# Kernel tuning notes

Hardware: AMD Instinct MI355X
Metric: run time of the kernel (lower is better)

The kernel has to match this reference:

```python
import jax, jax.numpy as jnp
import numpy as np
import math

B, CIN, COUT, K, R = 8, 128, 128, 7, 2
GC = 16                     # group_channels (init arg `groups`)
G = COUT // GC              # number of dynamic-weight groups = 8
H = W = 32
EPS = 1e-5


def c4_lift(w):
    # w: [o, i, 4] -> dense 1x1 weight [o*4, i*4] via cyclic C4 shifts
    # torch: weight[:, r] = w[..., roll-by-r]  (e.g. r=1 -> [3,0,1,2])
    Wr = jnp.stack([jnp.roll(w, r, axis=-1) for r in range(4)], axis=1)  # [o,4,i,4]
    o, _, i, _ = Wr.shape
    return Wr.reshape(o * 4, i * 4)


def setup_inputs() -> dict:
    key = jax.random.key(0)
    ks = jax.random.split(key, 4)
    sc = 1.0 / math.sqrt(4 * CIN / 2)
    x = jax.random.normal(ks[0], (B, CIN * 4, H, W), dtype=jnp.float32)
    v_w = jax.random.normal(ks[1], (COUT, CIN, 4), dtype=jnp.float32) * sc
    c1_w = jax.random.normal(ks[2], (CIN // R, CIN, 4), dtype=jnp.float32) * sc
    gn_g = jnp.ones((CIN // R * 4,), jnp.float32)
    gn_b = jnp.zeros((CIN // R * 4,), jnp.float32)
    c2_w = jax.random.normal(ks[3], (K * K * G, CIN // R), dtype=jnp.float32) * (1.0 / math.sqrt(CIN // R))
    c2_b = jnp.zeros((K * K * G,), jnp.float32)
    return {"x": x, "v_w": v_w, "c1_w": c1_w, "gn_g": gn_g, "gn_b": gn_b, "c2_w": c2_w, "c2_b": c2_b}


def _forward(x, v_w, c1_w, gn_g, gn_b, c2_w, c2_b):
    b, _, h, w = x.shape
    # conv1: C4-equivariant 1x1
    t = jnp.einsum('oc,bchw->bohw', c4_lift(c1_w), x)        # [b, (CIN//R)*4, h, w]
    # GroupNorm(num_groups=CIN//R) -> normalize each group of 4 channels over (4,h,w)
    tr = t.reshape(b, CIN // R, 4, h, w)
    mu = tr.mean(axis=(2, 3, 4), keepdims=True)
    var = tr.var(axis=(2, 3, 4), keepdims=True)
    t = ((tr - mu) * jax.lax.rsqrt(var + EPS)).reshape(b, CIN // R * 4, h, w)
    t = jax.nn.relu(t * gn_g[None, :, None, None] + gn_b[None, :, None, None])
    # conv2: Conv3d 1x1 over the (c, 4) view
    tv = t.reshape(b, CIN // R, 4, h, w)
    wmap = jnp.einsum('oc,bcrhw->borhw', c2_w, tv) + c2_b[None, :, None, None, None]
    wmap = wmap.reshape(b, G, K, K, 4, h, w)
    # rotate the KxK kernel by r*90deg for C4 element r (r=0 identity)
    wmap = jnp.stack([jnp.rot90(wmap[:, :, :, :, r], k=r, axes=(2, 3)) for r in range(4)], axis=4)
    wmap = wmap.reshape(b, G, K * K, 4, h, w)                 # [b, g, p, r, h, w]
    # v branch (C4 1x1) + unfold (im2col, pad (K-1)//2, stride 1)
    v = jnp.einsum('oc,bchw->bohw', c4_lift(v_w), x)          # [b, COUT*4, h, w]
    p = (K - 1) // 2
    vp = jnp.pad(v, ((0, 0), (0, 0), (p, p), (p, p)))
    patches = jnp.stack([vp[:, :, i:i + h, j:j + w] for i in range(K) for j in range(K)], axis=2)
    patches = patches.reshape(b, G, GC, 4, K * K, h, w)       # [b, g, c, r, p, h, w]
    out = jnp.einsum('bgprhw,bgcrphw->bgcrhw', wmap, patches)
    return out.reshape(b, COUT * 4, h, w)


def reference(x, v_w, c1_w, gn_g, gn_b, c2_w, c2_b):
    return _forward(x, v_w, c1_w, gn_g, gn_b, c2_w, c2_b)
```

## Files before the change

### kernel.cpp

```cpp
#include <hip/hip_runtime.h>

#define BB   8
#define CIN  128
#define COUT 128
#define KS   7
#define HH   32
#define WWID 32
#define HW   1024
#define NG   8
#define GC   16
#define MROWS 768
#define TROWS 256
#define VROWS 512
#define KDIM 512
#define WMAP_O 392
#define WMAP_OP 448
#define C2K  64

#define AS1 __attribute__((address_space(1)))
#define AS3 __attribute__((address_space(3)))

typedef __attribute__((ext_vector_type(8))) short bf16x8;
typedef __attribute__((ext_vector_type(4))) float f32x4;

__device__ __forceinline__ short f2bf(float f) {
    unsigned u = __builtin_bit_cast(unsigned, f);
    u += 0x7fff + ((u >> 16) & 1);
    return (short)(u >> 16);
}
__device__ __forceinline__ float bf2f(unsigned short u) {
    unsigned v = (unsigned)u << 16;
    return __builtin_bit_cast(float, v);
}

__global__ __launch_bounds__(256) void prep_kernel(
    const float* __restrict__ x, const float* __restrict__ v_w,
    const float* __restrict__ c1_w, const float* __restrict__ c2_w,
    const float* __restrict__ c2_b,
    short* __restrict__ XT, short* __restrict__ Wb,
    short* __restrict__ c2wb, float* __restrict__ c2bp,
    float* __restrict__ gnstat)
{
    __shared__ short t[64][66];
    int bx = blockIdx.x, tid = threadIdx.x;
    if (bx < 1024) {
        int b = bx >> 7, c0 = ((bx >> 4) & 7) * 64, n0 = (bx & 15) * 64;
        const float* xb = x + ((size_t)b * KDIM + c0) * HW + n0;
        #pragma unroll
        for (int l = 0; l < 16; ++l) {
            int flat = l * 256 + tid;
            int row = flat >> 6, col = flat & 63;
            t[col][row] = f2bf(xb[(size_t)row * HW + col]);
        }
        __syncthreads();
        short* xt = XT + ((size_t)b * HW + n0) * KDIM + c0;
        #pragma unroll
        for (int l = 0; l < 8; ++l) {
            int u = l * 256 + tid;
            int nrow = u >> 5, cp = (u & 31) * 2;
            short2 v = make_short2(t[nrow][cp], t[nrow][cp + 1]);
            *(short2*)(xt + (size_t)nrow * KDIM + cp) = v;
        }
    } else if (bx < 2560) {
        int idx = (bx - 1024) * 256 + tid;
        int row = idx >> 9, col = idx & 511;
        int i = col >> 2, s = col & 3;
        float val;
        if (row < 256) {
            int o = row >> 2, r = row & 3;
            val = c1_w[(o * CIN + i) * 4 + ((s - r) & 3)];
        } else {
            int ro = row - 256;
            int o = ro >> 2, r = ro & 3;
            val = v_w[(o * CIN + i) * 4 + ((s - r) & 3)];
        }
        Wb[idx] = f2bf(val);
    } else if (bx < 2672) {
        int idx = (bx - 2560) * 256 + tid;
        int o = idx >> 6, k = idx & 63;
        c2wb[idx] = f2bf(o < WMAP_O ? c2_w[o * C2K + k] : 0.f);
        if (idx < WMAP_OP)
            c2bp[idx] = idx < WMAP_O ? c2_b[idx] : 0.f;
    } else {
        *(float4*)(gnstat + tid * 4) = make_float4(0.f, 0.f, 0.f, 0.f);
    }
}

#define GBM 64
#define GBN 128
#define GBK 64
__global__ __launch_bounds__(256) void gemm_mfma_kernel(
    const short* __restrict__ Wb, const short* __restrict__ XT,
    short* __restrict__ tvb, float* __restrict__ gnstat)
{
    __shared__ short As[GBM * GBK];
    __shared__ short Bs[GBN * GBK];
    int b  = blockIdx.z;
    int m0 = blockIdx.y * GBM;
    int n0 = blockIdx.x * GBN;
    int tid = threadIdx.x;
    int lane = tid & 63, wv = tid >> 6;
    int wm = wv & 1, wn = wv >> 1;
    int rl = lane & 15, kg = lane >> 4;
    const short* Ab = Wb + (size_t)m0 * KDIM;
    const short* Bb = XT + ((size_t)b * HW + n0) * KDIM;
    f32x4 acc[2][4] = {};

    for (int k0 = 0; k0 < KDIM; k0 += GBK) {
        #pragma unroll
        for (int l = 0; l < 2; ++l) {
            int c = l * 256 + tid;
            int row = c >> 3, kc = c & 7;
            int kcs = kc ^ (row & 7);
            __builtin_amdgcn_global_load_lds(
                (const AS1 void*)(Ab + (size_t)row * KDIM + k0 + kcs * 8),
                (AS3 void*)(As + (l * 256 + wv * 64) * 8), 16, 0, 0);
        }
        #pragma unroll
        for (int l = 0; l < 4; ++l) {
            int c = l * 256 + tid;
            int row = c >> 3, kc = c & 7;
            int kcs = kc ^ (row & 7);
            __builtin_amdgcn_global_load_lds(
                (const AS1 void*)(Bb + (size_t)row * KDIM + k0 + kcs * 8),
                (AS3 void*)(Bs + (l * 256 + wv * 64) * 8), 16, 0, 0);
        }
        __syncthreads();
        #pragma unroll
        for (int ks = 0; ks < 2; ++ks) {
            bf16x8 af[2], bfr[4];
            #pragma unroll
            for (int mf = 0; mf < 2; ++mf) {
                int row = wm * 32 + mf * 16 + rl;
                af[mf] = *(const bf16x8*)(As + row * GBK + ((ks * 4 + kg) ^ (row & 7)) * 8);
            }
            #pragma unroll
            for (int nf = 0; nf < 4; ++nf) {
                int row = wn * 64 + nf * 16 + rl;
                bfr[nf] = *(const bf16x8*)(Bs + row * GBK + ((ks * 4 + kg) ^ (row & 7)) * 8);
            }
            #pragma unroll
            for (int mf = 0; mf < 2; ++mf)
                #pragma unroll
                for (int nf = 0; nf < 4; ++nf)
                    acc[mf][nf] = __builtin_amdgcn_mfma_f32_16x16x32_bf16(af[mf], bfr[nf], acc[mf][nf], 0, 0, 0);
        }
        __syncthreads();
    }

    short* Cb = tvb + (size_t)b * MROWS * HW;
    #pragma unroll
    for (int mf = 0; mf < 2; ++mf) {
        int rowb = m0 + wm * 32 + mf * 16 + kg * 4;
        #pragma unroll
        for (int nf = 0; nf < 4; ++nf) {
            int col = n0 + wn * 64 + nf * 16 + rl;
            #pragma unroll
            for (int i = 0; i < 4; ++i)
                Cb[(size_t)(rowb + i) * HW + col] = f2bf(acc[mf][nf][i]);
        }
    }

    if (m0 < TROWS) {
        #pragma unroll
        for (int mf = 0; mf < 2; ++mf) {
            float s = 0.f, sq = 0.f;
            #pragma unroll
            for (int nf = 0; nf < 4; ++nf)
                #pragma unroll
                for (int i = 0; i < 4; ++i) {
                    float v = acc[mf][nf][i];
                    s += v; sq += v * v;
                }
            #pragma unroll
            for (int m = 1; m <= 8; m <<= 1) {
                s  += __shfl_xor(s, m);
                sq += __shfl_xor(sq, m);
            }
            if (rl == 0) {
                int grp = (m0 + wm * 32 + mf * 16 + kg * 4) >> 2;
                atomicAdd(&gnstat[(b * 64 + grp) * 2],     s);
                atomicAdd(&gnstat[(b * 64 + grp) * 2 + 1], sq);
            }
        }
    }
}

__global__ __launch_bounds__(256) void tkn2_kernel(
    const short* __restrict__ tvb, const float* __restrict__ gnstat,
    const float* __restrict__ gn_g, const float* __restrict__ gn_b,
    short* __restrict__ tn)
{
    __shared__ short ts[64][72];
    __shared__ float sc[64], sh[64];
    int b4r = blockIdx.x;
    int b = b4r >> 2, r = b4r & 3;
    int hw0 = blockIdx.y * 64;
    int tid = threadIdx.x;
    if (tid < 64) {
        float s   = gnstat[(b * 64 + tid) * 2];
        float sq  = gnstat[(b * 64 + tid) * 2 + 1];
        float mu  = s * (1.f / 4096.f);
        float var = sq * (1.f / 4096.f) - mu * mu;
        float inv = rsqrtf(var + 1e-5f);
        int ch = tid * 4 + r;
        float g = gn_g[ch], bb = gn_b[ch];
        sc[tid] = inv * g;
        sh[tid] = bb - mu * inv * g;
    }
    #pragma unroll
    for (int l = 0; l < 16; ++l) {
        int flat = l * 256 + tid;
        int c = flat >> 6, hw = flat & 63;
        ts[c][hw] = tvb[((size_t)b * MROWS + c * 4 + r) * HW + hw0 + hw];
    }
    __syncthreads();
    #pragma unroll
    for (int l = 0; l < 2; ++l) {
        int u = l * 256 + tid;
        int hw = u >> 3, c0 = (u & 7) * 8;
        bf16x8 v;
        #pragma unroll
        for (int j = 0; j < 8; ++j) {
            float f = bf2f((unsigned short)ts[c0 + j][hw]);
            f = fmaxf(f * sc[c0 + j] + sh[c0 + j], 0.f);
            v[j] = f2bf(f);
        }
        *(bf16x8*)(tn + ((size_t)b4r * HW + hw0 + hw) * C2K + c0) = v;
    }
}

__global__ __launch_bounds__(256) void wmap3_kernel(
    const short* __restrict__ c2wb, const short* __restrict__ tn,
    const float* __restrict__ c2bp, short* __restrict__ wmapB)
{
    __shared__ short smem[64 * 64 + 128 * 64];
    short* As = smem;
    short* Bs = smem + 64 * 64;
    short* Ps = smem;
    int n0  = blockIdx.x * 128;
    int m0  = blockIdx.y * 64;
    int b4r = blockIdx.z;
    int tid = threadIdx.x;
    int lane = tid & 63, wv = tid >> 6;
    int wm = wv & 1, wn = wv >> 1;
    int rl = lane & 15, kg = lane >> 4;
    const short* Bb = tn + ((size_t)b4r * HW + n0) * C2K;

    #pragma unroll
    for (int l = 0; l < 2; ++l) {
        int c = l * 256 + tid;
        int row = c >> 3, kc = c & 7;
        int kcs = kc ^ (row & 7);
        __builtin_amdgcn_global_load_lds(
            (const AS1 void*)(c2wb + (size_t)(m0 + row) * C2K + kcs * 8),
            (AS3 void*)(As + (l * 256 + wv * 64) * 8), 16, 0, 0);
    }
    #pragma unroll
    for (int l = 0; l < 4; ++l) {
        int c = l * 256 + tid;
        int row = c >> 3, kc = c & 7;
        int kcs = kc ^ (row & 7);
        __builtin_amdgcn_global_load_lds(
            (const AS1 void*)(Bb + (size_t)row * C2K + kcs * 8),
            (AS3 void*)(Bs + (l * 256 + wv * 64) * 8), 16, 0, 0);
    }
    __syncthreads();

    f32x4 acc[2][4] = {};
    #pragma unroll
    for (int ks = 0; ks < 2; ++ks) {
        bf16x8 af[2], bfr[4];
        #pragma unroll
        for (int mf = 0; mf < 2; ++mf) {
            int row = wm * 32 + mf * 16 + rl;
            af[mf] = *(const bf16x8*)(As + row * 64 + ((ks * 4 + kg) ^ (row & 7)) * 8);
        }
        #pragma unroll
        for (int nf = 0; nf < 4; ++nf) {
            int row = wn * 64 + nf * 16 + rl;
            bfr[nf] = *(const bf16x8*)(Bs + row * 64 + ((ks * 4 + kg) ^ (row & 7)) * 8);
        }
        #pragma unroll
        for (int mf = 0; mf < 2; ++mf)
            #pragma unroll
            for (int nf = 0; nf < 4; ++nf)
                acc[mf][nf] = __builtin_amdgcn_mfma_f32_16x16x32_bf16(af[mf], bfr[nf], acc[mf][nf], 0, 0, 0);
    }
    __syncthreads();

    #pragma unroll
    for (int mf = 0; mf < 2; ++mf) {
        int rowl = wm * 32 + mf * 16 + kg * 4;
        float bi[4];
        #pragma unroll
        for (int i = 0; i < 4; ++i) bi[i] = c2bp[m0 + rowl + i];
        #pragma unroll
        for (int nf = 0; nf < 4; ++nf) {
            int col = wn * 64 + nf * 16 + rl;
            #pragma unroll
            for (int i = 0; i < 4; ++i)
                Ps[(rowl + i) * 136 + col] = f2bf(acc[mf][nf][i] + bi[i]);
        }
    }
    __syncthreads();

    int row = tid >> 2, segl = tid & 3;
    if (m0 + row < WMAP_O) {
        short* dst = wmapB + (size_t)b4r * WMAP_OP * HW + (size_t)(m0 + row) * HW + n0;
        #pragma unroll
        for (int s2 = 0; s2 < 4; ++s2) {
            int col = segl * 8 + s2 * 32;
            *(bf16x8*)(dst + col) = *(const bf16x8*)(Ps + row * 136 + col);
        }
    }
}

__global__ __launch_bounds__(256, 5) void agg7_kernel(
    const short* __restrict__ tvb, const short* __restrict__ wmapB,
    float* __restrict__ out)
{
    __shared__ float vt[16][10][44];
    int bx = blockIdx.x;
    int b = bx >> 5;
    int g = (bx >> 2) & 7;
    int r = bx & 3;
    int h0  = blockIdx.y * 4;
    int tid = threadIdx.x;
    int w0q = tid & 7, hl = (tid >> 3) & 3, cp = tid >> 5;
    int h = h0 + hl, w0 = w0q * 4;

    int A, Bc, Cc;
    if      (r == 0) { A = 0;  Bc = 7;  Cc = 1;  }
    else if (r == 1) { A = 6;  Bc = -1; Cc = 7;  }
    else if (r == 2) { A = 48; Bc = -7; Cc = -1; }
    else             { A = 42; Bc = 1;  Cc = -7; }

    const short* vpb = tvb + ((size_t)b * MROWS + TROWS) * HW;
    for (int e = tid; e < 480; e += 256) {
        int cc  = e / 30;
        int rem = e - cc * 30;
        int row = rem / 3, q = rem - row * 3;
        int col = (q == 0) ? 0 : (36 + (q - 1) * 4);
        *(float4*)(&vt[cc][row][col]) = make_float4(0.f, 0.f, 0.f, 0.f);
    }
    for (int f = tid; f < 1280; f += 256) {
        int cc  = f / 80;
        int rem = f - cc * 80;
        int row = rem >> 3, q = rem & 7;
        int gh = h0 - 3 + row;
        float4 v4 = make_float4(0.f, 0.f, 0.f, 0.f);
        if (gh >= 0 && gh < HH) {
            int ch = (g * GC + cc) * 4 + r;
            ushort4 u = *(const ushort4*)(vpb + (size_t)ch * HW + gh * WWID + q * 4);
            v4 = make_float4(bf2f(u.x), bf2f(u.y), bf2f(u.z), bf2f(u.w));
        }
        *(float4*)(&vt[cc][row][4 + q * 4]) = v4;
    }
    __syncthreads();

    const short* wmb = wmapB + ((size_t)(b * 4 + r) * WMAP_OP + g * 49) * HW + h * WWID + w0;
    float acc[2][4] = {};
    #pragma unroll
    for (int di = 0; di < 7; ++di) {
        float wrf[7][4];
        #pragma unroll
        for (int dj = 0; dj < 7; ++dj) {
            int porig = A + Bc * di + Cc * dj;
            ushort4 wv = *(const ushort4*)(wmb + (size_t)porig * HW);
            wrf[dj][0] = bf2f(wv.x); wrf[dj][1] = bf2f(wv.y);
            wrf[dj][2] = bf2f(wv.z); wrf[dj][3] = bf2f(wv.w);
        }
        #pragma unroll
        for (int c2 = 0; c2 < 2; ++c2) {
            int hc = cp * 2 + c2;
            const float* rp = &vt[hc][hl + di][w0];
            float4 q0 = *(const float4*)(rp);
            float4 q1 = *(const float4*)(rp + 4);
            float4 q2 = *(const float4*)(rp + 8);
            float win[12] = {q0.x, q0.y, q0.z, q0.w,
                             q1.x, q1.y, q1.z, q1.w,
                             q2.x, q2.y, q2.z, q2.w};
            #pragma unroll
            for (int dj = 0; dj < 7; ++dj)
                #pragma unroll
                for (int px = 0; px < 4; ++px)
                    acc[c2][px] += wrf[dj][px] * win[px + dj + 1];
        }
    }
    #pragma unroll
    for (int c2 = 0; c2 < 2; ++c2) {
        int ch = (g * GC + cp * 2 + c2) * 4 + r;
        float4 o4 = make_float4(acc[c2][0], acc[c2][1], acc[c2][2], acc[c2][3]);
        *(float4*)(out + ((size_t)b * 512 + ch) * HW + h * WWID + w0) = o4;
    }
}

extern "C" void kernel_launch(void* const* d_in, const int* in_sizes, int n_in,
                              void* d_out, int out_size, void* d_ws, size_t ws_size,
                              hipStream_t stream)
{
    const float* x    = (const float*)d_in[0];
    const float* v_w  = (const float*)d_in[1];
    const float* c1_w = (const float*)d_in[2];
    const float* gn_g = (const float*)d_in[3];
    const float* gn_b = (const float*)d_in[4];
    const float* c2_w = (const float*)d_in[5];
    const float* c2_b = (const float*)d_in[6];
    float* out = (float*)d_out;

    char* p = (char*)d_ws;
    short* Wb     = (short*)p;           p += (size_t)MROWS * KDIM * 2;
    short* tvb    = (short*)p;           p += (size_t)BB * MROWS * HW * 2;
    short* wmapB  = (short*)p;           p += (size_t)32 * WMAP_OP * HW * 2;
    short* XT     = (short*)wmapB;
    short* tn     = (short*)p;           p += (size_t)32 * HW * C2K * 2;
    short* c2wb   = (short*)p;           p += (size_t)WMAP_OP * C2K * 2;
    float* c2bp   = (float*)p;           p += (size_t)WMAP_OP * 4;
    float* gnstat = (float*)p;           p += (size_t)512 * 2 * 4;

    prep_kernel     <<<2673, 256, 0, stream>>>(x, v_w, c1_w, c2_w, c2_b, XT, Wb, c2wb, c2bp, gnstat);
    gemm_mfma_kernel<<<dim3(HW / GBN, MROWS / GBM, BB), 256, 0, stream>>>(Wb, XT, tvb, gnstat);
    tkn2_kernel     <<<dim3(32, 16), 256, 0, stream>>>(tvb, gnstat, gn_g, gn_b, tn);
    wmap3_kernel    <<<dim3(HW / 128, WMAP_OP / 64, 32), 256, 0, stream>>>(c2wb, tn, c2bp, wmapB);
    agg7_kernel     <<<dim3(BB * NG * 4, 8), 256, 0, stream>>>(tvb, wmapB, out);
}
```

Measured before the change: 62.68 us.

## Shrink GEMM N tile, stage C via LDS, retile aggregation by channel halves

The GEMM tile shrinks from 128 to 64 columns, which doubles the block count. Its epilogue now stages results through shared memory so each row is written to global memory as coalesced 16-byte vectors instead of scattered 2-byte stores. The aggregation kernel now covers 8 rows by 8 channels per block instead of 4 rows by 16 channels, split over a z dimension. This lowers the halo overhead per row, and each wmap load is reused across fewer channels but over more rows. The cost is an extra LDS round trip and barrier in the GEMM, and more total B-tile traffic from the smaller N tile.

```diff
diff --git a/kernel.cpp b/kernel.cpp
--- a/kernel.cpp
+++ b/kernel.cpp
@@ -87,24 +87,26 @@
 }
 
 #define GBM 64
-#define GBN 128
+#define GBN 64
 #define GBK 64
 __global__ __launch_bounds__(256) void gemm_mfma_kernel(
     const short* __restrict__ Wb, const short* __restrict__ XT,
     short* __restrict__ tvb, float* __restrict__ gnstat)
 {
-    __shared__ short As[GBM * GBK];
-    __shared__ short Bs[GBN * GBK];
+    __shared__ short smem[GBM * GBK + GBN * GBK];
+    short* As = smem;
+    short* Bs = smem + GBM * GBK;
+    short* Ps = smem;
     int b  = blockIdx.z;
     int m0 = blockIdx.y * GBM;
     int n0 = blockIdx.x * GBN;
     int tid = threadIdx.x;
     int lane = tid & 63, wv = tid >> 6;
-    int wm = wv & 1, wn = wv >> 1;
+    int wm = wv & 1, wn = (wv >> 1) & 1;
     int rl = lane & 15, kg = lane >> 4;
     const short* Ab = Wb + (size_t)m0 * KDIM;
     const short* Bb = XT + ((size_t)b * HW + n0) * KDIM;
-    f32x4 acc[2][4] = {};
+    f32x4 acc[2][2] = {};
 
     for (int k0 = 0; k0 < KDIM; k0 += GBK) {
         #pragma unroll
@@ -117,7 +119,7 @@
                 (AS3 void*)(As + (l * 256 + wv * 64) * 8), 16, 0, 0);
         }
         #pragma unroll
-        for (int l = 0; l < 4; ++l) {
+        for (int l = 0; l < 2; ++l) {
             int c = l * 256 + tid;
             int row = c >> 3, kc = c & 7;
             int kcs = kc ^ (row & 7);
@@ -128,37 +130,24 @@
         __syncthreads();
         #pragma unroll
         for (int ks = 0; ks < 2; ++ks) {
-            bf16x8 af[2], bfr[4];
+            bf16x8 af[2], bfr[2];
             #pragma unroll
             for (int mf = 0; mf < 2; ++mf) {
                 int row = wm * 32 + mf * 16 + rl;
                 af[mf] = *(const bf16x8*)(As + row * GBK + ((ks * 4 + kg) ^ (row & 7)) * 8);
             }
             #pragma unroll
-            for (int nf = 0; nf < 4; ++nf) {
-                int row = wn * 64 + nf * 16 + rl;
+            for (int nf = 0; nf < 2; ++nf) {
+                int row = wn * 32 + nf * 16 + rl;
                 bfr[nf] = *(const bf16x8*)(Bs + row * GBK + ((ks * 4 + kg) ^ (row & 7)) * 8);
             }
             #pragma unroll
             for (int mf = 0; mf < 2; ++mf)
                 #pragma unroll
-                for (int nf = 0; nf < 4; ++nf)
+                for (int nf = 0; nf < 2; ++nf)
                     acc[mf][nf] = __builtin_amdgcn_mfma_f32_16x16x32_bf16(af[mf], bfr[nf], acc[mf][nf], 0, 0, 0);
         }
         __syncthreads();
-    }
-
-    short* Cb = tvb + (size_t)b * MROWS * HW;
-    #pragma unroll
-    for (int mf = 0; mf < 2; ++mf) {
-        int rowb = m0 + wm * 32 + mf * 16 + kg * 4;
-        #pragma unroll
-        for (int nf = 0; nf < 4; ++nf) {
-            int col = n0 + wn * 64 + nf * 16 + rl;
-            #pragma unroll
-            for (int i = 0; i < 4; ++i)
-                Cb[(size_t)(rowb + i) * HW + col] = f2bf(acc[mf][nf][i]);
-        }
     }
 
     if (m0 < TROWS) {
@@ -166,7 +155,7 @@
         for (int mf = 0; mf < 2; ++mf) {
             float s = 0.f, sq = 0.f;
             #pragma unroll
-            for (int nf = 0; nf < 4; ++nf)
+            for (int nf = 0; nf < 2; ++nf)
                 #pragma unroll
                 for (int i = 0; i < 4; ++i) {
                     float v = acc[mf][nf][i];
@@ -182,6 +171,29 @@
                 atomicAdd(&gnstat[(b * 64 + grp) * 2],     s);
                 atomicAdd(&gnstat[(b * 64 + grp) * 2 + 1], sq);
             }
+        }
+    }
+
+    #pragma unroll
+    for (int mf = 0; mf < 2; ++mf) {
+        int rowl = wm * 32 + mf * 16 + kg * 4;
+        #pragma unroll
+        for (int nf = 0; nf < 2; ++nf) {
+            int col = wn * 32 + nf * 16 + rl;
+            #pragma unroll
+            for (int i = 0; i < 4; ++i)
+                Ps[(rowl + i) * 68 + col] = f2bf(acc[mf][nf][i]);
+        }
+    }
+    __syncthreads();
+
+    {
+        int row = tid >> 2, segl = tid & 3;
+        short* dst = tvb + (size_t)b * MROWS * HW + (size_t)(m0 + row) * HW + n0;
+        #pragma unroll
+        for (int s2 = 0; s2 < 2; ++s2) {
+            int col = segl * 8 + s2 * 32;
+            *(bf16x8*)(dst + col) = *(const bf16x8*)(Ps + row * 68 + col);
         }
     }
 }
@@ -316,18 +328,20 @@
     }
 }
 
-__global__ __launch_bounds__(256, 5) void agg7_kernel(
+__global__ __launch_bounds__(256, 5) void agg6_kernel(
     const short* __restrict__ tvb, const short* __restrict__ wmapB,
     float* __restrict__ out)
 {
-    __shared__ float vt[16][10][44];
+    __shared__ float vt[8][15][44];
     int bx = blockIdx.x;
     int b = bx >> 5;
     int g = (bx >> 2) & 7;
     int r = bx & 3;
-    int h0  = blockIdx.y * 4;
-    int tid = threadIdx.x;
-    int w0q = tid & 7, hl = (tid >> 3) & 3, cp = tid >> 5;
+    int h0   = blockIdx.y * 8;
+    int half = blockIdx.z;
+    int tid  = threadIdx.x;
+    int w0q = tid & 7, hb = (tid >> 3) & 1, cc4 = (tid >> 4) & 3, cq = tid >> 6;
+    int hl = cq * 2 + hb;
     int h = h0 + hl, w0 = w0q * 4;
 
     int A, Bc, Cc;
@@ -337,21 +351,21 @@
     else             { A = 42; Bc = 1;  Cc = -7; }
 
     const short* vpb = tvb + ((size_t)b * MROWS + TROWS) * HW;
-    for (int e = tid; e < 480; e += 256) {
-        int cc  = e / 30;
-        int rem = e - cc * 30;
+    for (int e = tid; e < 8 * 15 * 3; e += 256) {
+        int cc  = e / 45;
+        int rem = e - cc * 45;
         int row = rem / 3, q = rem - row * 3;
         int col = (q == 0) ? 0 : (36 + (q - 1) * 4);
         *(float4*)(&vt[cc][row][col]) = make_float4(0.f, 0.f, 0.f, 0.f);
     }
-    for (int f = tid; f < 1280; f += 256) {
-        int cc  = f / 80;
-        int rem = f - cc * 80;
+    for (int f = tid; f < 8 * 15 * 8; f += 256) {
+        int cc  = f / 120;
+        int rem = f - cc * 120;
         int row = rem >> 3, q = rem & 7;
         int gh = h0 - 3 + row;
         float4 v4 = make_float4(0.f, 0.f, 0.f, 0.f);
         if (gh >= 0 && gh < HH) {
-            int ch = (g * GC + cc) * 4 + r;
+            int ch = (g * GC + half * 8 + cc) * 4 + r;
             ushort4 u = *(const ushort4*)(vpb + (size_t)ch * HW + gh * WWID + q * 4);
             v4 = make_float4(bf2f(u.x), bf2f(u.y), bf2f(u.z), bf2f(u.w));
         }
@@ -373,7 +387,7 @@
         }
         #pragma unroll
         for (int c2 = 0; c2 < 2; ++c2) {
-            int hc = cp * 2 + c2;
+            int hc = cc4 * 2 + c2;
             const float* rp = &vt[hc][hl + di][w0];
             float4 q0 = *(const float4*)(rp);
             float4 q1 = *(const float4*)(rp + 4);
@@ -390,7 +404,7 @@
     }
     #pragma unroll
     for (int c2 = 0; c2 < 2; ++c2) {
-        int ch = (g * GC + cp * 2 + c2) * 4 + r;
+        int ch = (g * GC + half * 8 + cc4 * 2 + c2) * 4 + r;
         float4 o4 = make_float4(acc[c2][0], acc[c2][1], acc[c2][2], acc[c2][3]);
         *(float4*)(out + ((size_t)b * 512 + ch) * HW + h * WWID + w0) = o4;
     }
@@ -423,5 +437,5 @@
     gemm_mfma_kernel<<<dim3(HW / GBN, MROWS / GBM, BB), 256, 0, stream>>>(Wb, XT, tvb, gnstat);
     tkn2_kernel     <<<dim3(32, 16), 256, 0, stream>>>(tvb, gnstat, gn_g, gn_b, tn);
     wmap3_kernel    <<<dim3(HW / 128, WMAP_OP / 64, 32), 256, 0, stream>>>(c2wb, tn, c2bp, wmapB);
-    agg7_kernel     <<<dim3(BB * NG * 4, 8), 256, 0, stream>>>(tvb, wmapB, out);
-}
+    agg6_kernel     <<<dim3(BB * NG * 4, 4, 2), 256, 0, stream>>>(tvb, wmapB, out);
+}
```

Result: slower. 64.20 us (+2.4%).
